# Optimization experiments

Hardware: AMD Instinct MI355X
Metric: run time of the kernel (lower is better)

Reference implementation:

```python
import jax, jax.numpy as jnp
import numpy as np

EPS = 1e-5  # BatchNorm eps; eval mode with running_mean=0, running_var=1

def _bn(x, g, b):
    return x * (g / jnp.sqrt(1.0 + EPS)) + b

def _lrelu(x):
    return jnp.where(x >= 0, x, 0.2 * x)

def setup_inputs() -> dict:
    key = jax.random.key(0)
    ks = jax.random.split(key, 30)
    def w(i, shape, s=0.05):
        return jax.random.normal(ks[i], shape, dtype=jnp.float32) * s
    inp = {"x": jax.random.normal(ks[0], (8, 10, 4096), dtype=jnp.float32), "k": 20}
    inp.update(
        w1=w(1, (64, 9)),    g1=1.0 + w(2, (64,), 0.1),  b1=w(3, (64,), 0.1),
        w2=w(4, (64, 64)),   g2=1.0 + w(5, (64,), 0.1),  b2=w(6, (64,), 0.1),
        w3=w(7, (128, 128)), g3=1.0 + w(8, (128,), 0.1), b3=w(9, (128,), 0.1),
        w4=w(10, (256, 128)), g4=1.0 + w(11, (256,), 0.1), b4=w(12, (256,), 0.1),
        w5=w(13, (1024, 256)), g5=1.0 + w(14, (1024,), 0.1), b5=w(15, (1024,), 0.1),
        l1w=w(16, (512, 1472)), l1b=w(17, (512,), 0.1),
        g6=1.0 + w(18, (512,), 0.1), b6=w(19, (512,), 0.1),
        l2w=w(20, (256, 512)), l2b=w(21, (256,), 0.1),
        g7=1.0 + w(22, (256,), 0.1), b7=w(23, (256,), 0.1),
        l3w=w(24, (2, 256)), l3b=w(25, (2,), 0.1),
    )
    return inp

def reference(x, k, w1, g1, b1, w2, g2, b2, w3, g3, b3, w4, g4, b4, w5, g5, b5,
              l1w, l1b, g6, b6, l2w, l2b, g7, b7, l3w, l3b):
    B, C, N = x.shape
    # --- kNN on xyz (first 3 channels); topk of negative squared distance ---
    xyz = x[:, :3, :]
    xx = jnp.sum(xyz * xyz, axis=1)                        # [B,N]
    inner = jnp.einsum('bcn,bcm->bnm', xyz, xyz)           # [B,N,N]
    pd = 2.0 * inner - xx[:, :, None] - xx[:, None, :]     # -||xi-xj||^2
    idx = jax.lax.top_k(pd, k)[1]                          # [B,N,k]
    # --- neighbor gather + edge features (xyz_i, rgb_i, rgb_i - rgb_j) ---
    xt = jnp.transpose(x, (0, 2, 1))                       # [B,N,C]
    nbr = xt[jnp.arange(B)[:, None, None], idx]            # [B,N,k,C]
    xyz_i = jnp.broadcast_to(xt[:, :, None, :3], (B, N, k, 3))
    rgb_i = jnp.broadcast_to(xt[:, :, None, 3:6], (B, N, k, 3))
    f = jnp.concatenate([xyz_i, rgb_i, rgb_i - nbr[..., 3:6]], axis=-1)  # [B,N,k,9]
    # --- EdgeConv MLPs (1x1 convs) + max over neighbors ---
    h = _lrelu(_bn(jnp.einsum('bnkc,oc->bnko', f, w1), g1, b1))
    h = _lrelu(_bn(jnp.einsum('bnkc,oc->bnko', h, w2), g2, b2))
    x1 = jnp.max(h, axis=2)                                # [B,N,64]
    x2 = _lrelu(_bn(jnp.einsum('bnc,oc->bno', jnp.concatenate([x1, x1], -1), w3), g3, b3))  # [B,N,128]
    x3 = _lrelu(_bn(jnp.einsum('bnc,oc->bno', x2, w4), g4, b4))  # [B,N,256]
    x4 = jnp.max(x3, axis=1)                               # [B,256] global max pool
    # conv5 applied to x4 repeated over N; max over identical copies == itself
    xg = _lrelu(_bn(x4 @ w5.T, g5, b5))                    # [B,1024]
    feat = jnp.concatenate([jnp.broadcast_to(xg[:, None, :], (B, N, 1024)), x3, x2, x1], axis=-1)  # [B,N,1472]
    h = _lrelu(_bn(feat @ l1w.T + l1b, g6, b6))            # dropout = identity (eval)
    h = _lrelu(_bn(h @ l2w.T + l2b, g7, b7))
    out = h @ l3w.T + l3b                                  # [B,N,num_classes]
    return jnp.transpose(out, (0, 2, 1))                   # [B,num_classes,N]
```

## Files before the change

### kernel.cpp

```cpp
#include <hip/hip_runtime.h>


#define KNN 20
#define NPID 32768
#define RS 0.99999500003750f

#define X3_PO 8388608
#define X2_PO 4194304
#define X1_PO 2097152

typedef unsigned short ushort_t;
typedef unsigned int u32;
typedef __attribute__((ext_vector_type(8))) short bf16x8;
typedef __attribute__((ext_vector_type(4))) float f32x4;

#define LDS_PTR(p) ((__attribute__((address_space(3))) void*)(p))
#define GLB_PTR(p) ((const __attribute__((address_space(1))) void*)(p))

__device__ __forceinline__ float lrelu(float z) { return z >= 0.f ? z : 0.2f * z; }
__device__ __forceinline__ unsigned short f2bf(float f) {
  unsigned int u = __float_as_uint(f);
  return (unsigned short)((u + 0x7fffu + ((u >> 16) & 1u)) >> 16);
}
__device__ __forceinline__ float bf2f(unsigned short h) { return __uint_as_float((unsigned int)h << 16); }
__device__ __forceinline__ u32 pack2(u32 e0, u32 e1) { return (e1 << 16) | (e0 & 0xffffu); }
__device__ __forceinline__ u32 encf(float f) {
  const u32 u = __float_as_uint(f);
  return (u >> 31) ? ~u : (u | 0x80000000u);
}
__device__ __forceinline__ float decf(u32 e) {
  return __uint_as_float((e >> 31) ? (e ^ 0x80000000u) : ~e);
}
__device__ __forceinline__ f32x4 mfma16(uint4 a, uint4 b, f32x4 c) {
  return __builtin_amdgcn_mfma_f32_16x16x32_bf16(
      __builtin_bit_cast(bf16x8, a), __builtin_bit_cast(bf16x8, b), c, 0, 0, 0);
}

__global__ __launch_bounds__(256) void xyzw_kernel(const float* __restrict__ x, float4* __restrict__ xyzw) {
  const int i = blockIdx.x * 256 + threadIdx.x;
  const int b = i >> 12, n = i & 4095;
  const float* xb = x + (size_t)b * 40960;
  const float px = xb[n], py = xb[4096 + n], pz = xb[8192 + n];
  const float xx = __fadd_rn(__fadd_rn(__fmul_rn(px, px), __fmul_rn(py, py)), __fmul_rn(pz, pz));
  float4 v; v.x = px; v.y = py; v.z = pz; v.w = xx;
  xyzw[i] = v;
}

__global__ __launch_bounds__(256, 3) void knn_kernel(const float4* __restrict__ xyzw, int* __restrict__ idxo) {
  __shared__ __align__(16) float4 pt[2048];
  __shared__ float cval[8][64];
  __shared__ int cidx[8][64];
  const int tid = threadIdx.x, lane = tid & 63, wave = tid >> 6;
  const int qbase = blockIdx.x * 8 + wave * 2;
  const int b = qbase >> 12;
  const float4* xw = xyzw + ((size_t)b << 12);
  const int nA = qbase & 4095;
  const float4 PA = xw[nA];
  const float4 PB = xw[nA + 1];
  float2 d[64];
  float lmaxA = -3.4e38f, lmaxB = -3.4e38f;
#pragma unroll
  for (int t = 0; t < 2; ++t) {
    if (t) __syncthreads();
#pragma unroll
    for (int r = 0; r < 8; ++r) {
      const int chunk = wave * 8 + r;
      __builtin_amdgcn_global_load_lds(GLB_PTR(xw + t * 2048 + chunk * 64 + lane),
                                       LDS_PTR((char*)pt + chunk * 1024), 16, 0, 0);
    }
    __syncthreads();
#pragma unroll
    for (int jj = 0; jj < 32; ++jj) {
      const float4 Q = pt[jj * 64 + lane];
      const float iA = __fadd_rn(__fadd_rn(__fmul_rn(PA.x, Q.x), __fmul_rn(PA.y, Q.y)), __fmul_rn(PA.z, Q.z));
      const float pdA = __fsub_rn(__fsub_rn(__fmul_rn(2.0f, iA), PA.w), Q.w);
      const float iB = __fadd_rn(__fadd_rn(__fmul_rn(PB.x, Q.x), __fmul_rn(PB.y, Q.y)), __fmul_rn(PB.z, Q.z));
      const float pdB = __fsub_rn(__fsub_rn(__fmul_rn(2.0f, iB), PB.w), Q.w);
      d[t * 32 + jj].x = pdA;
      d[t * 32 + jj].y = pdB;
      lmaxA = fmaxf(lmaxA, pdA);
      lmaxB = fmaxf(lmaxB, pdB);
    }
  }
  float t0q[2];
#pragma unroll
  for (int q = 0; q < 2; ++q) {
    float v = q ? lmaxB : lmaxA;
#pragma unroll
    for (int k = 2; k <= 64; k <<= 1) {
#pragma unroll
      for (int j = k >> 1; j > 0; j >>= 1) {
        const float ov = __shfl_xor(v, j, 64);
        const bool keepMax = (((lane & k) == 0) == ((lane & j) == 0));
        v = keepMax ? fmaxf(v, ov) : fminf(v, ov);
      }
    }
    t0q[q] = __shfl(v, 19, 64);
  }
  int Cq[2];
#pragma unroll
  for (int q = 0; q < 2; ++q) {
    const float t0 = t0q[q];
    int base = 0;
#pragma unroll
    for (int j = 0; j < 64; ++j) {
      const float dv = q ? d[j].y : d[j].x;
      const bool take = (dv >= t0);
      const unsigned long long mk = __ballot(take);
      if (take) {
        const int pos = base + __popcll(mk & ((1ull << lane) - 1ull));
        if (pos < 64) {
          cval[wave * 2 + q][pos] = dv;
          cidx[wave * 2 + q][pos] = (j << 6) + lane;
        }
      }
      base += (int)__popcll(mk);
    }
    Cq[q] = base;
  }
  int* outA = idxo + (size_t)qbase * KNN;
  if (Cq[0] <= 32 && Cq[1] <= 32) {
    const int qsel = lane >> 5, c = lane & 31;
    const int row = wave * 2 + qsel;
    const int Cc = qsel ? Cq[1] : Cq[0];
    unsigned long long key = 0ull;
    if (c < Cc) {
      key = ((unsigned long long)encf(cval[row][c]) << 32) |
            (unsigned long long)(0xFFFFFFFFu - (unsigned int)cidx[row][c]);
    }
#pragma unroll
    for (int k = 2; k <= 32; k <<= 1) {
#pragma unroll
      for (int j = k >> 1; j > 0; j >>= 1) {
        const unsigned long long ok = (unsigned long long)__shfl_xor((long long)key, j, 64);
        const bool keepMax = (((c & k) == 0) == ((c & j) == 0));
        key = (keepMax == (key > ok)) ? key : ok;
      }
    }
    if (c < KNN) outA[qsel * KNN + c] = (int)(0xFFFFFFFFu - (unsigned int)key);
  } else {
#pragma unroll
    for (int q = 0; q < 2; ++q) {
      int* out = outA + q * KNN;
      const int C = Cq[q];
      if (C <= 64) {
        unsigned long long key = 0ull;
        if (lane < C) {
          key = ((unsigned long long)encf(cval[wave * 2 + q][lane]) << 32) |
                (unsigned long long)(0xFFFFFFFFu - (unsigned int)cidx[wave * 2 + q][lane]);
        }
#pragma unroll
        for (int k = 2; k <= 64; k <<= 1) {
#pragma unroll
          for (int j = k >> 1; j > 0; j >>= 1) {
            const unsigned long long ok = (unsigned long long)__shfl_xor((long long)key, j, 64);
            const bool keepMax = (((lane & k) == 0) == ((lane & j) == 0));
            key = (keepMax == (key > ok)) ? key : ok;
          }
        }
        if (lane < KNN) out[lane] = (int)(0xFFFFFFFFu - (unsigned int)key);
      } else {
        unsigned long long used = 0ull;
#pragma unroll 1
        for (int it = 0; it < KNN; ++it) {
          float lv = -3.4e38f;
          int li = 1 << 30;
#pragma unroll
          for (int j = 0; j < 64; ++j) {
            const float dv = q ? d[j].y : d[j].x;
            if (!((used >> j) & 1ull) && dv > lv) {
              lv = dv;
              li = (j << 6) + lane;
            }
          }
          float bv = lv;
          int bi = li;
#pragma unroll
          for (int s = 1; s < 64; s <<= 1) {
            const float ovv = __shfl_xor(bv, s, 64);
            const int oii = __shfl_xor(bi, s, 64);
            if (ovv > bv || (ovv == bv && oii < bi)) { bv = ovv; bi = oii; }
          }
          if (lane == 0) out[it] = bi;
          if ((bi & 63) == lane) used |= 1ull << (bi >> 6);
        }
      }
    }
  }
}

__global__ __launch_bounds__(256) void edge_kernel(const float* __restrict__ x, const int* __restrict__ idxi,
    const float* __restrict__ w1, const float* __restrict__ g1, const float* __restrict__ b1,
    const ushort_t* __restrict__ w2p, const float* __restrict__ g2, const float* __restrict__ b2,
    ushort_t* __restrict__ x1o) {
  __shared__ u32 hstage[4][16][64];
  const int tid = threadIdx.x, lane = tid & 63, wave = tid >> 6;
  const int fr = lane & 15, kg = lane >> 4;
  const int pbase = blockIdx.x * 64 + wave * 16;
  const int b = (blockIdx.x * 64) >> 12;
  const float* xq = x + (size_t)b * 40960;

  const int nA = (pbase + fr) & 4095;
  float cv[6]; ushort_t chv[6], clv[6];
#pragma unroll
  for (int j = 0; j < 6; ++j) {
    cv[j] = xq[j * 4096 + nA];
    chv[j] = f2bf(cv[j]);
    clv[j] = f2bf(cv[j] - bf2f(chv[j]));
  }
  const float crv = cv[3], cgv = cv[4], cbv = cv[5];

  u32 aC0 = 0, aC1 = 0, aC2 = 0, aC3 = 0;
  if (kg == 0) { aC0 = pack2(chv[0], chv[1]); aC1 = pack2(chv[2], chv[3]); aC2 = pack2(chv[4], chv[5]); }
  else if (kg == 1) { aC0 = (u32)chv[0] << 16; aC1 = pack2(chv[1], chv[2]); aC2 = pack2(chv[3], chv[4]); aC3 = chv[5]; }
  else if (kg == 2) { aC1 = pack2(clv[0], clv[1]); aC2 = pack2(clv[2], clv[3]); aC3 = pack2(clv[4], clv[5]); }

  float s1v[4], t1v[4], s2v[4], t2v[4];
#pragma unroll
  for (int fj = 0; fj < 4; ++fj) {
    const int och = fj * 16 + fr;
    s1v[fj] = g1[och] * RS; t1v[fj] = b1[och];
    s2v[fj] = g2[och] * RS; t2v[fj] = b2[och];
  }

  uint4 w1Bv[4];
#pragma unroll
  for (int fj = 0; fj < 4; ++fj) {
    const int och = fj * 16 + fr;
    ushort_t wh[9], wl[9];
#pragma unroll
    for (int j = 0; j < 9; ++j) {
      const float wv = w1[och * 9 + j];
      wh[j] = f2bf(wv);
      wl[j] = f2bf(wv - bf2f(wh[j]));
    }
    uint4 q;
    if (kg == 0)      { q.x = pack2(wh[0], wh[1]); q.y = pack2(wh[2], wh[3]); q.z = pack2(wh[4], wh[5]); q.w = pack2(wh[6], wh[7]); }
    else if (kg == 1) { q.x = pack2(wh[8], wl[0]); q.y = pack2(wl[1], wl[2]); q.z = pack2(wl[3], wl[4]); q.w = pack2(wl[5], wl[6]); }
    else if (kg == 2) { q.x = pack2(wl[7], wl[8]); q.y = pack2(wh[0], wh[1]); q.z = pack2(wh[2], wh[3]); q.w = pack2(wh[4], wh[5]); }
    else              { q.x = pack2(wh[6], wh[7]); q.y = pack2(wh[8], 0);     q.z = 0;                   q.w = 0; }
    w1Bv[fj] = q;
  }

  uint4 w2Bh[4][2], w2Bl[4][2];
#pragma unroll
  for (int fj = 0; fj < 4; ++fj) {
    const int och = fj * 16 + fr;
#pragma unroll
    for (int sub = 0; sub < 2; ++sub) {
      const ushort_t* ph = w2p + och * 64 + sub * 32 + kg * 8;
      w2Bh[fj][sub] = *(const uint4*)ph;
      w2Bl[fj][sub] = *(const uint4*)(ph + 4096);
    }
  }

  const int prow = (pbase + fr) * KNN;
  int miA = idxi[prow];
  int miN = idxi[prow + 1];
  float pr = xq[12288 + miA], pg = xq[16384 + miA], pb = xq[20480 + miA];

  f32x4 xm[4];
#pragma unroll
  for (int fj = 0; fj < 4; ++fj) { xm[fj][0] = -3.4e38f; xm[fj][1] = -3.4e38f; xm[fj][2] = -3.4e38f; xm[fj][3] = -3.4e38f; }
  const f32x4 zz = {0.f, 0.f, 0.f, 0.f};

#pragma unroll 1
  for (int kk = 0; kk < KNN; ++kk) {
    const float nrv = pr, ngv = pg, nbv = pb;
    if (kk < KNN - 1) { pr = xq[12288 + miN]; pg = xq[16384 + miN]; pb = xq[20480 + miN]; }
    if (kk < KNN - 2) { miN = idxi[prow + kk + 2]; }

    const float dr = crv - nrv, dg = cgv - ngv, db = cbv - nbv;
    const ushort_t drh = f2bf(dr), dgh = f2bf(dg), dbh = f2bf(db);
    const ushort_t drl = f2bf(dr - bf2f(drh)), dgl = f2bf(dg - bf2f(dgh)), dbl = f2bf(db - bf2f(dbh));

    uint4 aF;
    if (kg == 0)      { aF.x = aC0; aF.y = aC1; aF.z = aC2; aF.w = pack2(drh, dgh); }
    else if (kg == 1) { aF.x = aC0 | dbh; aF.y = aC1; aF.z = aC2; aF.w = aC3 | ((u32)drh << 16); }
    else if (kg == 2) { aF.x = pack2(dgh, dbh); aF.y = aC1; aF.z = aC2; aF.w = aC3; }
    else              { aF.x = pack2(drl, dgl); aF.y = (u32)dbl; aF.z = 0; aF.w = 0; }

    f32x4 h1a[4];
#pragma unroll
    for (int fj = 0; fj < 4; ++fj) h1a[fj] = mfma16(aF, w1Bv[fj], zz);

#pragma unroll
    for (int fj = 0; fj < 4; ++fj)
#pragma unroll
      for (int r = 0; r < 4; ++r) {
        float z = h1a[fj][r] * s1v[fj] + t1v[fj];
        z = fmaxf(z, 0.2f * z);
        const ushort_t hi = f2bf(z), lo = f2bf(z - bf2f(hi));
        const int pC = kg * 4 + r;
        hstage[wave][pC][(fj * 16 + fr) ^ ((pC & 7) << 3)] = ((u32)hi << 16) | lo;
      }

    f32x4 a2[4] = {zz, zz, zz, zz};
#pragma unroll
    for (int sub = 0; sub < 2; ++sub) {
      const u32* rp = &hstage[wave][fr][(sub * 32 + kg * 8) ^ ((fr & 7) << 3)];
      const uint4 q0 = *(const uint4*)rp;
      const uint4 q1 = *(const uint4*)(rp + 4);
      uint4 ah, al;
      ah.x = __builtin_amdgcn_perm(q0.y, q0.x, 0x07060302u); al.x = __builtin_amdgcn_perm(q0.y, q0.x, 0x05040100u);
      ah.y = __builtin_amdgcn_perm(q0.w, q0.z, 0x07060302u); al.y = __builtin_amdgcn_perm(q0.w, q0.z, 0x05040100u);
      ah.z = __builtin_amdgcn_perm(q1.y, q1.x, 0x07060302u); al.z = __builtin_amdgcn_perm(q1.y, q1.x, 0x05040100u);
      ah.w = __builtin_amdgcn_perm(q1.w, q1.z, 0x07060302u); al.w = __builtin_amdgcn_perm(q1.w, q1.z, 0x05040100u);
#pragma unroll
      for (int fj = 0; fj < 4; ++fj) {
        a2[fj] = mfma16(ah, w2Bh[fj][sub], a2[fj]);
        a2[fj] = mfma16(ah, w2Bl[fj][sub], a2[fj]);
        a2[fj] = mfma16(al, w2Bh[fj][sub], a2[fj]);
      }
    }

#pragma unroll
    for (int fj = 0; fj < 4; ++fj)
#pragma unroll
      for (int r = 0; r < 4; ++r) {
        float z = a2[fj][r] * s2v[fj] + t2v[fj];
        z = fmaxf(z, 0.2f * z);
        xm[fj][r] = fmaxf(xm[fj][r], z);
      }
  }

#pragma unroll
  for (int fj = 0; fj < 4; ++fj)
#pragma unroll
    for (int r = 0; r < 4; ++r) {
      const size_t e = (size_t)(pbase + kg * 4 + r) * 64 + fj * 16 + fr;
      const float v = xm[fj][r];
      const ushort_t hi = f2bf(v);
      x1o[e] = hi;
      x1o[X1_PO + e] = f2bf(v - bf2f(hi));
    }
}

__global__ __launch_bounds__(256) void prep_kernel(const float* __restrict__ w3, const float* __restrict__ w4,
    const float* __restrict__ l1w, const float* __restrict__ l2w, const float* __restrict__ w2,
    ushort_t* __restrict__ w3fp, ushort_t* __restrict__ w4p,
    ushort_t* __restrict__ l1wp, ushort_t* __restrict__ l2wp, ushort_t* __restrict__ w2p,
    u32* __restrict__ x4u) {
  const int i = blockIdx.x * 256 + threadIdx.x;
  float f; ushort_t* hp; int n, j;
  if (i < 8192) {
    const int o = i >> 6, c = i & 63;
    f = w3[o * 128 + c] + w3[o * 128 + 64 + c];
    hp = w3fp; n = 8192; j = i;
  } else if (i < 8192 + 32768) {
    j = i - 8192; f = w4[j]; hp = w4p; n = 32768;
  } else if (i < 8192 + 32768 + 131072) {
    j = i - 8192 - 32768; f = l2w[j]; hp = l2wp; n = 131072;
  } else if (i < 172032 + 229376) {
    j = i - 172032;
    const int row = j / 448, col = j - row * 448;
    f = l1w[row * 1472 + 1024 + col];
    hp = l1wp; n = 229376;
  } else if (i < 401408 + 4096) {
    j = i - 401408; f = w2[j]; hp = w2p; n = 4096;
  } else if (i < 405504 + 2048) {
    x4u[i - 405504] = 0u;
    return;
  } else return;
  const unsigned short h = f2bf(f);
  hp[j] = h;
  hp[n + j] = f2bf(f - bf2f(h));
}

template <int MODE, int OUTF32, int DOMAX>
__global__ __launch_bounds__(256) void gemm_bf16(
    const ushort_t* __restrict__ A, const ushort_t* __restrict__ W, void* __restrict__ outv,
    const int Ktot, const int Nout, const int n_tiles,
    const int aPO, const int wPO, const int outPO,
    const float* __restrict__ gg, const float* __restrict__ bb,
    const float* __restrict__ linb, const int do_lrelu,
    const float* __restrict__ ybp, const ushort_t* __restrict__ x3,
    const ushort_t* __restrict__ x2, const ushort_t* __restrict__ x1,
    u32* __restrict__ x4u) {
  __shared__ __align__(16) ushort_t lds[16384];
  const int tid = threadIdx.x, lane = tid & 63, wid = tid >> 6;
  const int nwg = gridDim.x;
  int id = (blockIdx.x & 7) * (nwg >> 3) + (blockIdx.x >> 3);
  const int mt = id / n_tiles, nt = id - mt * n_tiles;
  const int m0 = mt * 128, o0 = nt * 128;
  const int fr = lane & 15, kg = lane >> 4;
  const int wr = wid >> 1, wc = wid & 1;
  int rA[4], rB[4];
#pragma unroll
  for (int i = 0; i < 4; ++i) { rA[i] = wr * 64 + i * 16 + fr; rB[i] = wc * 64 + i * 16 + fr; }
  f32x4 acc[4][4] = {};
  const ushort_t* srcB = (wid == 2) ? W : W + wPO;
  const ushort_t* srcA0 = (MODE == 0) ? ((wid == 0) ? A : A + aPO) : nullptr;
  const int pl = (wid == 1);

  for (int kc = 0; kc < Ktot; kc += 32) {
#pragma unroll
    for (int c = 0; c < 8; ++c) {
      const int row = c * 16 + (lane >> 2);
      const int rslot = (lane & 3) ^ ((row >> 1) & 3);
      const int k = kc + rslot * 8;
      const ushort_t* q;
      if (wid >= 2) {
        q = srcB + (size_t)(o0 + row) * Ktot + k;
      } else if (MODE == 0) {
        q = srcA0 + (size_t)(m0 + row) * Ktot + k;
      } else {
        const int m = m0 + row;
        if (k < 256)      q = x3 + pl * X3_PO + (size_t)m * 256 + k;
        else if (k < 384) q = x2 + pl * X2_PO + (size_t)m * 128 + (k - 256);
        else              q = x1 + pl * X1_PO + (size_t)m * 64 + (k - 384);
      }
      __builtin_amdgcn_global_load_lds(GLB_PTR(q), LDS_PTR(&lds[wid * 4096 + c * 512]), 16, 0, 0);
    }
    __syncthreads();
    bf16x8 ah[4], al[4], bh[4], bl[4];
#pragma unroll
    for (int i = 0; i < 4; ++i) {
      const int off = rA[i] * 32 + ((kg ^ ((rA[i] >> 1) & 3)) << 3);
      ah[i] = *(const bf16x8*)&lds[off];
      al[i] = *(const bf16x8*)&lds[4096 + off];
    }
#pragma unroll
    for (int j = 0; j < 4; ++j) {
      const int off = rB[j] * 32 + ((kg ^ ((rB[j] >> 1) & 3)) << 3);
      bh[j] = *(const bf16x8*)&lds[8192 + off];
      bl[j] = *(const bf16x8*)&lds[12288 + off];
    }
#pragma unroll
    for (int i = 0; i < 4; ++i)
#pragma unroll
      for (int j = 0; j < 4; ++j) {
        acc[i][j] = __builtin_amdgcn_mfma_f32_16x16x32_bf16(ah[i], bh[j], acc[i][j], 0, 0, 0);
        acc[i][j] = __builtin_amdgcn_mfma_f32_16x16x32_bf16(ah[i], bl[j], acc[i][j], 0, 0, 0);
        acc[i][j] = __builtin_amdgcn_mfma_f32_16x16x32_bf16(al[i], bh[j], acc[i][j], 0, 0, 0);
      }
    __syncthreads();
  }
  float s[4], t[4];
#pragma unroll
  for (int j = 0; j < 4; ++j) {
    const int o = o0 + wc * 64 + j * 16 + fr;
    s[j] = gg[o] * RS;
    float add = linb ? linb[o] : 0.f;
    if (MODE == 1) add += ybp[((m0 >> 12) << 9) + o];
    t[j] = bb[o] + add * s[j];
  }
  float cm[4] = {-3.4e38f, -3.4e38f, -3.4e38f, -3.4e38f};
#pragma unroll
  for (int i = 0; i < 4; ++i) {
#pragma unroll
    for (int j = 0; j < 4; ++j) {
      const int col = o0 + wc * 64 + j * 16 + fr;
#pragma unroll
      for (int r = 0; r < 4; ++r) {
        const int row = m0 + wr * 64 + i * 16 + kg * 4 + r;
        float z = acc[i][j][r] * s[j] + t[j];
        if (do_lrelu) z = lrelu(z);
        if (DOMAX) cm[j] = fmaxf(cm[j], z);
        if (OUTF32) {
          ((float*)outv)[(size_t)row * Nout + col] = z;
        } else {
          ushort_t* oh = (ushort_t*)outv;
          const unsigned short h = f2bf(z);
          oh[(size_t)row * Nout + col] = h;
          oh[outPO + (size_t)row * Nout + col] = f2bf(z - bf2f(h));
        }
      }
    }
  }
  if (DOMAX) {
    __syncthreads();
    u32* mcol = (u32*)lds;
    if (tid < 128) mcol[tid] = 0u;
    __syncthreads();
#pragma unroll
    for (int j = 0; j < 4; ++j) atomicMax(&mcol[wc * 64 + j * 16 + fr], encf(cm[j]));
    __syncthreads();
    if (tid < 128) atomicMax(&x4u[((m0 >> 12) << 8) + o0 + tid], mcol[tid]);
  }
}

__global__ __launch_bounds__(256) void xg_kernel(const u32* __restrict__ x4u, const float* __restrict__ w5,
    const float* __restrict__ g5, const float* __restrict__ b5, float* __restrict__ xgf) {
  const int lane = threadIdx.x & 63, wave = threadIdx.x >> 6;
  const int o = blockIdx.x * 4 + wave;
  const int b = o >> 10, oc = o & 1023;
  const uint4 xu = *(const uint4*)&x4u[b * 256 + lane * 4];
  const float4 w = *(const float4*)&w5[(size_t)oc * 256 + lane * 4];
  float acc = decf(xu.x) * w.x + decf(xu.y) * w.y + decf(xu.z) * w.z + decf(xu.w) * w.w;
#pragma unroll
  for (int s = 1; s < 64; s <<= 1) acc += __shfl_xor(acc, s, 64);
  if (lane == 0) xgf[o] = lrelu(acc * (g5[oc] * RS) + b5[oc]);
}

__global__ __launch_bounds__(256) void yb_kernel(const float* __restrict__ xgf, const float* __restrict__ l1w,
    float* __restrict__ yb) {
  const int lane = threadIdx.x & 63, wave = threadIdx.x >> 6;
  const int o = blockIdx.x * 4 + wave;
  const int b = o >> 9, oc = o & 511;
  float acc = 0.f;
#pragma unroll
  for (int i = 0; i < 4; ++i) {
    const int k = i * 256 + lane * 4;
    const float4 w = *(const float4*)&l1w[(size_t)oc * 1472 + k];
    const float4 g = *(const float4*)&xgf[b * 1024 + k];
    acc += w.x * g.x + w.y * g.y + w.z * g.z + w.w * g.w;
  }
#pragma unroll
  for (int s = 1; s < 64; s <<= 1) acc += __shfl_xor(acc, s, 64);
  if (lane == 0) yb[o] = acc;
}

__global__ __launch_bounds__(256) void l3_kernel(const float* __restrict__ h6, const float* __restrict__ l3w,
    const float* __restrict__ l3b, float* __restrict__ out) {
  __shared__ float wl[512];
  const int tid = threadIdx.x;
  wl[tid] = l3w[tid]; wl[256 + tid] = l3w[256 + tid];
  __syncthreads();
  const int m = blockIdx.x * 256 + tid;
  float a0 = 0.f, a1 = 0.f;
#pragma unroll
  for (int c = 0; c < 256; c += 4) {
    const float4 h = *(const float4*)(h6 + (size_t)m * 256 + c);
    a0 += h.x * wl[c] + h.y * wl[c + 1] + h.z * wl[c + 2] + h.w * wl[c + 3];
    a1 += h.x * wl[256 + c] + h.y * wl[256 + c + 1] + h.z * wl[256 + c + 2] + h.w * wl[256 + c + 3];
  }
  const int b = m >> 12, n = m & 4095;
  out[(size_t)b * 8192 + n] = a0 + l3b[0];
  out[(size_t)b * 8192 + 4096 + n] = a1 + l3b[1];
}

extern "C" void kernel_launch(void* const* d_in, const int* in_sizes, int n_in,
                              void* d_out, int out_size, void* d_ws, size_t ws_size,
                              hipStream_t stream) {
  const float* x   = (const float*)d_in[0];
  const float* w1  = (const float*)d_in[2];
  const float* g1  = (const float*)d_in[3];
  const float* b1  = (const float*)d_in[4];
  const float* w2  = (const float*)d_in[5];
  const float* g2  = (const float*)d_in[6];
  const float* b2  = (const float*)d_in[7];
  const float* w3  = (const float*)d_in[8];
  const float* g3  = (const float*)d_in[9];
  const float* b3  = (const float*)d_in[10];
  const float* w4  = (const float*)d_in[11];
  const float* g4  = (const float*)d_in[12];
  const float* b4  = (const float*)d_in[13];
  const float* w5  = (const float*)d_in[14];
  const float* g5  = (const float*)d_in[15];
  const float* b5  = (const float*)d_in[16];
  const float* l1w = (const float*)d_in[17];
  const float* l1b = (const float*)d_in[18];
  const float* g6  = (const float*)d_in[19];
  const float* b6  = (const float*)d_in[20];
  const float* l2w = (const float*)d_in[21];
  const float* l2b = (const float*)d_in[22];
  const float* g7  = (const float*)d_in[23];
  const float* b7  = (const float*)d_in[24];
  const float* l3w = (const float*)d_in[25];
  const float* l3b = (const float*)d_in[26];
  float* outp = (float*)d_out;

  char* ws = (char*)d_ws;
  int*      idx  = (int*)(ws + 0);
  ushort_t* x1   = (ushort_t*)(ws + 2621440);
  ushort_t* x2   = (ushort_t*)(ws + 11010048);
  ushort_t* x3   = (ushort_t*)(ws + 27787264);
  ushort_t* w2p  = (ushort_t*)(ws + 61341696);
  u32*      x4u  = (u32*)(ws + 61358080);
  float*    xgf  = (float*)(ws + 61407232);
  float*    ybp  = (float*)(ws + 61448192);
  ushort_t* w3fp = (ushort_t*)(ws + 61440000);
  ushort_t* w4p  = (ushort_t*)(ws + 61472768);
  ushort_t* l2wp = (ushort_t*)(ws + 61603840);
  ushort_t* l1wp = (ushort_t*)(ws + 62128128);
  ushort_t* h5   = (ushort_t*)(ws + 65142784);
  float4*   xyzw = (float4*)(ws + 132251648);
  float*    h6   = (float*)(ws + 11010048);

  xyzw_kernel<<<128, 256, 0, stream>>>(x, xyzw);
  knn_kernel<<<NPID / 8, 256, 0, stream>>>(xyzw, idx);
  prep_kernel<<<1592, 256, 0, stream>>>(w3, w4, l1w, l2w, w2, w3fp, w4p, l1wp, l2wp, w2p, x4u);
  edge_kernel<<<NPID / 64, 256, 0, stream>>>(x, idx, w1, g1, b1, w2p, g2, b2, x1);
  gemm_bf16<0, 0, 0><<<256, 256, 0, stream>>>(x1, w3fp, x2, 64, 128, 1, X1_PO, 8192, X2_PO,
                                              g3, b3, nullptr, 1, nullptr, nullptr, nullptr, nullptr, nullptr);
  gemm_bf16<0, 0, 1><<<512, 256, 0, stream>>>(x2, w4p, x3, 128, 256, 2, X2_PO, 32768, X3_PO,
                                              g4, b4, nullptr, 1, nullptr, nullptr, nullptr, nullptr, x4u);
  xg_kernel<<<2048, 256, 0, stream>>>(x4u, w5, g5, b5, xgf);
  yb_kernel<<<1024, 256, 0, stream>>>(xgf, l1w, ybp);
  gemm_bf16<1, 0, 0><<<1024, 256, 0, stream>>>(nullptr, l1wp, h5, 448, 512, 4, 0, 229376, 16777216,
                                               g6, b6, l1b, 1, ybp, x3, x2, x1, nullptr);
  gemm_bf16<0, 1, 0><<<512, 256, 0, stream>>>(h5, l2wp, h6, 512, 256, 2, 16777216, 131072, 0,
                                              g7, b7, l2b, 1, nullptr, nullptr, nullptr, nullptr, nullptr);
  l3_kernel<<<128, 256, 0, stream>>>(h6, l3w, l3b, outp);
}
```

Baseline: 250.8 us.

## Enlarge kNN blocks to stage all points in LDS once and merge per-query sorts

The kNN kernel now uses 512-thread blocks that handle 16 queries. Each block loads all 4096 points of the batch into LDS in a single pass, so the two-stage load with its extra barrier goes away and each staged point is reused across twice as many queries. The threshold bitonic sort for the two queries of a wave now runs in one 32-lane sort per half-wave, after a cross-half max, and the two candidate ballot loops are interleaved. The cost is 64KB+ of LDS per block, which may limit how many blocks fit on a CU.

New measurement: 272.5 us. 1.09x slower.

```diff
diff --git a/kernel.cpp b/kernel.cpp
--- a/kernel.cpp
+++ b/kernel.cpp
@@ -46,83 +46,83 @@
   xyzw[i] = v;
 }
 
-__global__ __launch_bounds__(256, 3) void knn_kernel(const float4* __restrict__ xyzw, int* __restrict__ idxo) {
-  __shared__ __align__(16) float4 pt[2048];
-  __shared__ float cval[8][64];
-  __shared__ int cidx[8][64];
+__global__ __launch_bounds__(512, 4) void knn_kernel(const float4* __restrict__ xyzw, int* __restrict__ idxo) {
+  __shared__ __align__(16) float4 pt[4096];
+  __shared__ float cval[16][64];
+  __shared__ int cidx[16][64];
   const int tid = threadIdx.x, lane = tid & 63, wave = tid >> 6;
-  const int qbase = blockIdx.x * 8 + wave * 2;
+  const int qbase = blockIdx.x * 16 + wave * 2;
   const int b = qbase >> 12;
   const float4* xw = xyzw + ((size_t)b << 12);
+#pragma unroll
+  for (int r = 0; r < 8; ++r) {
+    const int chunk = wave * 8 + r;
+    __builtin_amdgcn_global_load_lds(GLB_PTR(xw + chunk * 64 + lane),
+                                     LDS_PTR((char*)pt + chunk * 1024), 16, 0, 0);
+  }
   const int nA = qbase & 4095;
   const float4 PA = xw[nA];
   const float4 PB = xw[nA + 1];
+  __syncthreads();
   float2 d[64];
   float lmaxA = -3.4e38f, lmaxB = -3.4e38f;
 #pragma unroll
-  for (int t = 0; t < 2; ++t) {
-    if (t) __syncthreads();
-#pragma unroll
-    for (int r = 0; r < 8; ++r) {
-      const int chunk = wave * 8 + r;
-      __builtin_amdgcn_global_load_lds(GLB_PTR(xw + t * 2048 + chunk * 64 + lane),
-                                       LDS_PTR((char*)pt + chunk * 1024), 16, 0, 0);
-    }
-    __syncthreads();
-#pragma unroll
-    for (int jj = 0; jj < 32; ++jj) {
-      const float4 Q = pt[jj * 64 + lane];
-      const float iA = __fadd_rn(__fadd_rn(__fmul_rn(PA.x, Q.x), __fmul_rn(PA.y, Q.y)), __fmul_rn(PA.z, Q.z));
-      const float pdA = __fsub_rn(__fsub_rn(__fmul_rn(2.0f, iA), PA.w), Q.w);
-      const float iB = __fadd_rn(__fadd_rn(__fmul_rn(PB.x, Q.x), __fmul_rn(PB.y, Q.y)), __fmul_rn(PB.z, Q.z));
-      const float pdB = __fsub_rn(__fsub_rn(__fmul_rn(2.0f, iB), PB.w), Q.w);
-      d[t * 32 + jj].x = pdA;
-      d[t * 32 + jj].y = pdB;
-      lmaxA = fmaxf(lmaxA, pdA);
-      lmaxB = fmaxf(lmaxB, pdB);
-    }
-  }
-  float t0q[2];
-#pragma unroll
-  for (int q = 0; q < 2; ++q) {
-    float v = q ? lmaxB : lmaxA;
-#pragma unroll
-    for (int k = 2; k <= 64; k <<= 1) {
-#pragma unroll
-      for (int j = k >> 1; j > 0; j >>= 1) {
-        const float ov = __shfl_xor(v, j, 64);
-        const bool keepMax = (((lane & k) == 0) == ((lane & j) == 0));
-        v = keepMax ? fmaxf(v, ov) : fminf(v, ov);
-      }
-    }
-    t0q[q] = __shfl(v, 19, 64);
-  }
-  int Cq[2];
-#pragma unroll
-  for (int q = 0; q < 2; ++q) {
-    const float t0 = t0q[q];
-    int base = 0;
-#pragma unroll
-    for (int j = 0; j < 64; ++j) {
-      const float dv = q ? d[j].y : d[j].x;
-      const bool take = (dv >= t0);
-      const unsigned long long mk = __ballot(take);
-      if (take) {
-        const int pos = base + __popcll(mk & ((1ull << lane) - 1ull));
-        if (pos < 64) {
-          cval[wave * 2 + q][pos] = dv;
-          cidx[wave * 2 + q][pos] = (j << 6) + lane;
-        }
-      }
-      base += (int)__popcll(mk);
-    }
-    Cq[q] = base;
-  }
+  for (int j = 0; j < 64; ++j) {
+    const float4 Q = pt[j * 64 + lane];
+    const float iA = __fadd_rn(__fadd_rn(__fmul_rn(PA.x, Q.x), __fmul_rn(PA.y, Q.y)), __fmul_rn(PA.z, Q.z));
+    const float pdA = __fsub_rn(__fsub_rn(__fmul_rn(2.0f, iA), PA.w), Q.w);
+    const float iB = __fadd_rn(__fadd_rn(__fmul_rn(PB.x, Q.x), __fmul_rn(PB.y, Q.y)), __fmul_rn(PB.z, Q.z));
+    const float pdB = __fsub_rn(__fsub_rn(__fmul_rn(2.0f, iB), PB.w), Q.w);
+    d[j].x = pdA;
+    d[j].y = pdB;
+    lmaxA = fmaxf(lmaxA, pdA);
+    lmaxB = fmaxf(lmaxB, pdB);
+  }
+  const float fA = fmaxf(lmaxA, __shfl_xor(lmaxA, 32, 64));
+  const float fB = fmaxf(lmaxB, __shfl_xor(lmaxB, 32, 64));
+  const int ch = lane & 31;
+  float v = (lane < 32) ? fA : fB;
+#pragma unroll
+  for (int k = 2; k <= 32; k <<= 1) {
+#pragma unroll
+    for (int j = k >> 1; j > 0; j >>= 1) {
+      const float ov = __shfl_xor(v, j, 64);
+      const bool keepMax = (((ch & k) == 0) == ((ch & j) == 0));
+      v = keepMax ? fmaxf(v, ov) : fminf(v, ov);
+    }
+  }
+  const float t0A = __shfl(v, 19, 64);
+  const float t0B = __shfl(v, 32 + 19, 64);
+  int baseA = 0, baseB = 0;
+#pragma unroll
+  for (int j = 0; j < 64; ++j) {
+    const bool takeA = (d[j].x >= t0A);
+    const unsigned long long mkA = __ballot(takeA);
+    if (takeA) {
+      const int pos = baseA + __popcll(mkA & ((1ull << lane) - 1ull));
+      if (pos < 64) {
+        cval[wave * 2][pos] = d[j].x;
+        cidx[wave * 2][pos] = (j << 6) + lane;
+      }
+    }
+    baseA += (int)__popcll(mkA);
+    const bool takeB = (d[j].y >= t0B);
+    const unsigned long long mkB = __ballot(takeB);
+    if (takeB) {
+      const int pos = baseB + __popcll(mkB & ((1ull << lane) - 1ull));
+      if (pos < 64) {
+        cval[wave * 2 + 1][pos] = d[j].y;
+        cidx[wave * 2 + 1][pos] = (j << 6) + lane;
+      }
+    }
+    baseB += (int)__popcll(mkB);
+  }
+  const int Cq0 = baseA, Cq1 = baseB;
   int* outA = idxo + (size_t)qbase * KNN;
-  if (Cq[0] <= 32 && Cq[1] <= 32) {
+  if (Cq0 <= 32 && Cq1 <= 32) {
     const int qsel = lane >> 5, c = lane & 31;
     const int row = wave * 2 + qsel;
-    const int Cc = qsel ? Cq[1] : Cq[0];
+    const int Cc = qsel ? Cq1 : Cq0;
     unsigned long long key = 0ull;
     if (c < Cc) {
       key = ((unsigned long long)encf(cval[row][c]) << 32) |
@@ -142,7 +142,7 @@
 #pragma unroll
     for (int q = 0; q < 2; ++q) {
       int* out = outA + q * KNN;
-      const int C = Cq[q];
+      const int C = q ? Cq1 : Cq0;
       if (C <= 64) {
         unsigned long long key = 0ull;
         if (lane < C) {
@@ -579,7 +579,7 @@
   float*    h6   = (float*)(ws + 11010048);
 
   xyzw_kernel<<<128, 256, 0, stream>>>(x, xyzw);
-  knn_kernel<<<NPID / 8, 256, 0, stream>>>(xyzw, idx);
+  knn_kernel<<<NPID / 16, 512, 0, stream>>>(xyzw, idx);
   prep_kernel<<<1592, 256, 0, stream>>>(w3, w4, l1w, l2w, w2, w3fp, w4p, l1wp, l2wp, w2p, x4u);
   edge_kernel<<<NPID / 64, 256, 0, stream>>>(x, idx, w1, g1, b1, w2p, g2, b2, x1);
   gemm_bf16<0, 0, 0><<<256, 256, 0, stream>>>(x1, w3fp, x2, 64, 128, 1, X1_PO, 8192, X2_PO,
```
